# Performance work log

Hardware: AMD Instinct MI355X
Metric: run time of the kernel (lower is better)

## Reference

```python
import jax, jax.numpy as jnp
import numpy as np
from jax import lax

DN = ('NCDHW', 'OIDHW', 'NCDHW')

def _reflect_conv(s, w, pad_dhw):
    # s: [B,2,D,H,W]; reflect-pad spatial dims then VALID conv -> same spatial size
    p = jnp.pad(s, ((0, 0), (0, 0)) + pad_dhw, mode='reflect')
    return lax.conv_general_dilated(p, w, window_strides=(1, 1, 1),
                                    padding='VALID', dimension_numbers=DN)

def setup_inputs() -> dict:
    key = jax.random.key(0)
    k = jax.random.split(key, 5)
    x = jax.random.normal(k[0], (4, 32, 16, 128, 128), dtype=jnp.float32)
    w1 = jax.random.normal(k[1], (1, 2, 7, 7, 5), dtype=jnp.float32) * 0.1
    w2 = jax.random.normal(k[2], (1, 2, 5, 5, 3), dtype=jnp.float32) * 0.1
    w3 = jax.random.normal(k[3], (1, 2, 3, 3, 1), dtype=jnp.float32) * 0.2
    wf = jax.random.normal(k[4], (1, 3, 1, 1, 1), dtype=jnp.float32) * 0.5
    return {'x': x, 'w1': w1, 'w2': w2, 'w3': w3, 'wf': wf}

def reference(x, w1, w2, w3, wf):
    # channel pool: mean & max over channel dim -> [B,2,D,H,W]
    s_in = jnp.concatenate([jnp.mean(x, axis=1, keepdims=True),
                            jnp.max(x, axis=1, keepdims=True)], axis=1)
    # branch pads in (D,H,W) order match kernels (7,7,5)/(5,5,3)/(3,3,1)
    s1 = _reflect_conv(s_in, w1, ((3, 3), (3, 3), (2, 2)))
    s2 = _reflect_conv(s_in, w2, ((2, 2), (2, 2), (1, 1)))
    s3 = _reflect_conv(s_in, w3, ((1, 1), (1, 1), (0, 0)))
    s = jnp.concatenate([s1, s2, s3], axis=1)  # [B,3,D,H,W]
    fused = lax.conv_general_dilated(s, wf, window_strides=(1, 1, 1),
                                     padding='VALID', dimension_numbers=DN)
    spatial_weight = jax.nn.sigmoid(fused)  # [B,1,D,H,W]
    return x * spatial_weight
```

## Files before the change

kernel.cpp:

```cpp
#include <hip/hip_runtime.h>
#include <math.h>

#define B_ 4
#define C_ 32
#define D_ 16
#define H_ 128
#define W_ 128
#define HW_ (H_*W_)
#define SP_ (D_*HW_)

typedef float f32x4 __attribute__((ext_vector_type(4)));

__device__ __forceinline__ int refl(int i, int n) {
    i = (i < 0) ? -i : i;
    i = (i >= n) ? (2*n - 2 - i) : i;
    return i;
}

__global__ void prep_weights_kernel(const float* __restrict__ w1,
                                    const float* __restrict__ w2,
                                    const float* __restrict__ w3,
                                    const float* __restrict__ wf,
                                    float* __restrict__ Wc) {
    int t = blockIdx.x * blockDim.x + threadIdx.x;
    if (t >= 2*7*7*5) return;
    int ow = t % 5;
    int oh = (t / 5) % 7;
    int od = (t / 35) % 7;
    int ci = t / 245;
    float v = wf[0] * w1[((ci*7+od)*7+oh)*5+ow];
    if (od>=1 && od<=5 && oh>=1 && oh<=5 && ow>=1 && ow<=3)
        v = fmaf(wf[1], w2[((ci*5+(od-1))*5+(oh-1))*3+(ow-1)], v);
    if (od>=2 && od<=4 && oh>=2 && oh<=4 && ow==2)
        v = fmaf(wf[2], w3[(ci*3+(od-2))*3+(oh-2)], v);
    Wc[t] = v;
}

__global__ __launch_bounds__(256) void pool_kernel(const float* __restrict__ x,
                                                   float* __restrict__ s) {
    int t = blockIdx.x * blockDim.x + threadIdx.x;
    if (t >= B_*D_*H_*(W_/4)) return;
    int w4 = (t % (W_/4)) * 4;
    int rest = t / (W_/4);
    int h = rest % H_;
    int bd = rest / H_;
    int d = bd % D_;
    int b = bd / D_;
    const float* xp = x + (b*C_*D_ + d)*HW_ + h*W_ + w4;
    f32x4 v = *(const f32x4*)xp;
    float sx=v.x, sy=v.y, sz=v.z, sw=v.w;
    float mx=v.x, my=v.y, mz=v.z, mw=v.w;
    #pragma unroll 4
    for (int c = 1; c < C_; ++c) {
        f32x4 u = *(const f32x4*)(xp + c*SP_);
        sx+=u.x; sy+=u.y; sz+=u.z; sw+=u.w;
        mx=fmaxf(mx,u.x); my=fmaxf(my,u.y); mz=fmaxf(mz,u.z); mw=fmaxf(mw,u.w);
    }
    const float inv = 1.0f/32.0f;
    float* sm = s + ((b*2+0)*D_ + d)*HW_ + h*W_ + w4;
    float* sM = s + ((b*2+1)*D_ + d)*HW_ + h*W_ + w4;
    f32x4 a; a.x=sx*inv; a.y=sy*inv; a.z=sz*inv; a.w=sw*inv;
    f32x4 m; m.x=mx; m.y=my; m.z=mz; m.w=mw;
    *(f32x4*)sm = a;
    *(f32x4*)sM = m;
}

__global__ __launch_bounds__(256) void spatial_att_kernel(
        const float* __restrict__ x,
        const float* __restrict__ s,
        const float* __restrict__ Wc,
        float* __restrict__ out) {
    int bid = blockIdx.x;
    int ht = bid & 15;
    int d0 = (bid >> 4) & 15;
    int b  = bid >> 8;
    int t = threadIdx.x;
    int lane = t & 63;
    int w0 = (t & 31) * 4;
    int h0 = ht * 8 + (t >> 5);

    const bool le = (t & 31) == 0;
    const bool re = (t & 31) == 31;

    int drow[7];
    #pragma unroll
    for (int od = 0; od < 7; ++od) drow[od] = refl(d0 + od - 3, D_) * HW_;

    float acc[4] = {0.f, 0.f, 0.f, 0.f};

    for (int ci = 0; ci < 2; ++ci) {
        const float* sc = s + (b*2 + ci)*SP_;
        const float* wcb_ci = Wc + ci*245;
        for (int oh = 0; oh < 7; ++oh) {
            const float* sh = sc + refl(h0 + oh - 3, H_)*W_ + w0;
            const float* wcb = wcb_ci + oh*5;
            #pragma unroll
            for (int od = 0; od < 7; ++od) {
                const f32x4 vv = *(const f32x4*)(sh + drow[od]);
                float lz = __shfl(vv.z, lane - 1);
                float lw = __shfl(vv.w, lane - 1);
                float rx = __shfl(vv.x, lane + 1);
                float ry = __shfl(vv.y, lane + 1);
                float v[8];
                v[0] = le ? vv.z : lz;
                v[1] = le ? vv.y : lw;
                v[2] = vv.x; v[3] = vv.y; v[4] = vv.z; v[5] = vv.w;
                v[6] = re ? vv.z : rx;
                v[7] = re ? vv.y : ry;
                const float* wp = wcb + od*35;
                #pragma unroll
                for (int ow = 0; ow < 5; ++ow) {
                    float wgt = wp[ow];
                    #pragma unroll
                    for (int wi = 0; wi < 4; ++wi)
                        acc[wi] = fmaf(wgt, v[wi+ow], acc[wi]);
                }
            }
        }
    }

    float sg[4];
    #pragma unroll
    for (int wi = 0; wi < 4; ++wi)
        sg[wi] = 1.0f/(1.0f + __expf(-acc[wi]));

    int obase = (b*C_*D_ + d0)*HW_ + h0*W_ + w0;
    #pragma unroll 4
    for (int c = 0; c < C_; ++c) {
        int i0 = obase + c*SP_;
        f32x4 xv = *(const f32x4*)(x + i0);
        f32x4 o; o.x=xv.x*sg[0]; o.y=xv.y*sg[1]; o.z=xv.z*sg[2]; o.w=xv.w*sg[3];
        __builtin_nontemporal_store(o, (f32x4*)(out + i0));
    }
}

extern "C" void kernel_launch(void* const* d_in, const int* in_sizes, int n_in,
                              void* d_out, int out_size, void* d_ws, size_t ws_size,
                              hipStream_t stream) {
    const float* x  = (const float*)d_in[0];
    const float* w1 = (const float*)d_in[1];
    const float* w2 = (const float*)d_in[2];
    const float* w3 = (const float*)d_in[3];
    const float* wf = (const float*)d_in[4];
    float* out = (float*)d_out;
    float* Wc = (float*)d_ws;
    float* s  = (float*)d_ws + 512;

    prep_weights_kernel<<<1, 512, 0, stream>>>(w1, w2, w3, wf, Wc);
    pool_kernel<<<(B_*D_*H_*(W_/4) + 255)/256, 256, 0, stream>>>(x, s);
    spatial_att_kernel<<<B_*D_*(H_/8), 256, 0, stream>>>(x, s, Wc, out);
}
```

Before: 88.57 us.

## Split stencil and multiply into separate kernels; use overlapping loads instead of shuffles

The fused stencil+multiply kernel is split in two. A stencil kernel writes a sigmoid gate map to workspace, and a separate multiply kernel spreads the 32-channel x*gate pass across 8x more blocks, so bandwidth-bound work gets more parallelism. Inside the stencil, cross-lane shuffles are replaced by two overlapping vector loads per row, and the pool loop now uses vector adds with a larger unroll. The cost is an extra launch plus a small gate-map write and read.

```diff
diff --git a/kernel.cpp b/kernel.cpp
--- a/kernel.cpp
+++ b/kernel.cpp
@@ -32,7 +32,7 @@
     if (od>=1 && od<=5 && oh>=1 && oh<=5 && ow>=1 && ow<=3)
         v = fmaf(wf[1], w2[((ci*5+(od-1))*5+(oh-1))*3+(ow-1)], v);
     if (od>=2 && od<=4 && oh>=2 && oh<=4 && ow==2)
-        v = fmaf(wf[2], w3[(ci*3+(od-2))*3+(oh-2)], v);
+        v = fmaf(wf[2], w3[(ci*3+(od-2))*3+(ow==2?(oh-2):0)], v);
     Wc[t] = v;
 }
 
@@ -48,39 +48,34 @@
     int b = bd / D_;
     const float* xp = x + (b*C_*D_ + d)*HW_ + h*W_ + w4;
     f32x4 v = *(const f32x4*)xp;
-    float sx=v.x, sy=v.y, sz=v.z, sw=v.w;
-    float mx=v.x, my=v.y, mz=v.z, mw=v.w;
-    #pragma unroll 4
+    f32x4 sm = v, mx = v;
+    #pragma unroll 8
     for (int c = 1; c < C_; ++c) {
         f32x4 u = *(const f32x4*)(xp + c*SP_);
-        sx+=u.x; sy+=u.y; sz+=u.z; sw+=u.w;
-        mx=fmaxf(mx,u.x); my=fmaxf(my,u.y); mz=fmaxf(mz,u.z); mw=fmaxf(mw,u.w);
+        sm += u;
+        mx.x=fmaxf(mx.x,u.x); mx.y=fmaxf(mx.y,u.y); mx.z=fmaxf(mx.z,u.z); mx.w=fmaxf(mx.w,u.w);
     }
-    const float inv = 1.0f/32.0f;
-    float* sm = s + ((b*2+0)*D_ + d)*HW_ + h*W_ + w4;
-    float* sM = s + ((b*2+1)*D_ + d)*HW_ + h*W_ + w4;
-    f32x4 a; a.x=sx*inv; a.y=sy*inv; a.z=sz*inv; a.w=sw*inv;
-    f32x4 m; m.x=mx; m.y=my; m.z=mz; m.w=mw;
-    *(f32x4*)sm = a;
-    *(f32x4*)sM = m;
+    sm *= (1.0f/32.0f);
+    *(f32x4*)(s + ((b*2+0)*D_ + d)*HW_ + h*W_ + w4) = sm;
+    *(f32x4*)(s + ((b*2+1)*D_ + d)*HW_ + h*W_ + w4) = mx;
 }
 
-__global__ __launch_bounds__(256) void spatial_att_kernel(
-        const float* __restrict__ x,
+__global__ __launch_bounds__(256) void stencil_kernel(
         const float* __restrict__ s,
         const float* __restrict__ Wc,
-        float* __restrict__ out) {
+        float* __restrict__ sg) {
     int bid = blockIdx.x;
     int ht = bid & 15;
     int d0 = (bid >> 4) & 15;
     int b  = bid >> 8;
     int t = threadIdx.x;
-    int lane = t & 63;
     int w0 = (t & 31) * 4;
     int h0 = ht * 8 + (t >> 5);
 
     const bool le = (t & 31) == 0;
     const bool re = (t & 31) == 31;
+    const int offL = le ? 0 : -2;
+    const int offR = re ? 0 :  2;
 
     int drow[7];
     #pragma unroll
@@ -96,17 +91,18 @@
             const float* wcb = wcb_ci + oh*5;
             #pragma unroll
             for (int od = 0; od < 7; ++od) {
-                const f32x4 vv = *(const f32x4*)(sh + drow[od]);
-                float lz = __shfl(vv.z, lane - 1);
-                float lw = __shfl(vv.w, lane - 1);
-                float rx = __shfl(vv.x, lane + 1);
-                float ry = __shfl(vv.y, lane + 1);
+                const float* rp = sh + drow[od];
+                const f32x4 L = *(const f32x4*)(rp + offL);
+                const f32x4 R = *(const f32x4*)(rp + offR);
                 float v[8];
-                v[0] = le ? vv.z : lz;
-                v[1] = le ? vv.y : lw;
-                v[2] = vv.x; v[3] = vv.y; v[4] = vv.z; v[5] = vv.w;
-                v[6] = re ? vv.z : rx;
-                v[7] = re ? vv.y : ry;
+                v[0] = le ? L.z : L.x;
+                v[1] = L.y;
+                v[2] = le ? L.x : L.z;
+                v[3] = le ? L.y : L.w;
+                v[4] = re ? R.z : R.x;
+                v[5] = re ? R.w : R.y;
+                v[6] = R.z;
+                v[7] = re ? R.y : R.w;
                 const float* wp = wcb + od*35;
                 #pragma unroll
                 for (int ow = 0; ow < 5; ++ow) {
@@ -119,18 +115,35 @@
         }
     }
 
-    float sg[4];
+    f32x4 o;
+    o.x = 1.0f/(1.0f + __expf(-acc[0]));
+    o.y = 1.0f/(1.0f + __expf(-acc[1]));
+    o.z = 1.0f/(1.0f + __expf(-acc[2]));
+    o.w = 1.0f/(1.0f + __expf(-acc[3]));
+    *(f32x4*)(sg + ((b*D_ + d0)*H_ + h0)*W_ + w0) = o;
+}
+
+__global__ __launch_bounds__(256) void mult_kernel(
+        const float* __restrict__ x,
+        const float* __restrict__ sg,
+        float* __restrict__ out) {
+    int bid = blockIdx.x;
+    int h = bid & 127;
+    int d = (bid >> 7) & 15;
+    int b = bid >> 11;
+    int t = threadIdx.x;
+    int w4 = (t & 31) * 4;
+    int c0 = t >> 5;
+
+    f32x4 g = *(const f32x4*)(sg + ((b*D_ + d)*H_ + h)*W_ + w4);
+
+    int base = (b*C_*D_ + d)*HW_ + h*W_ + w4;
     #pragma unroll
-    for (int wi = 0; wi < 4; ++wi)
-        sg[wi] = 1.0f/(1.0f + __expf(-acc[wi]));
-
-    int obase = (b*C_*D_ + d0)*HW_ + h0*W_ + w0;
-    #pragma unroll 4
-    for (int c = 0; c < C_; ++c) {
-        int i0 = obase + c*SP_;
+    for (int k = 0; k < 4; ++k) {
+        int c = c0 + k*8;
+        int i0 = base + c*SP_;
         f32x4 xv = *(const f32x4*)(x + i0);
-        f32x4 o; o.x=xv.x*sg[0]; o.y=xv.y*sg[1]; o.z=xv.z*sg[2]; o.w=xv.w*sg[3];
-        __builtin_nontemporal_store(o, (f32x4*)(out + i0));
+        __builtin_nontemporal_store(xv * g, (f32x4*)(out + i0));
     }
 }
 
@@ -145,8 +158,10 @@
     float* out = (float*)d_out;
     float* Wc = (float*)d_ws;
     float* s  = (float*)d_ws + 512;
+    float* sg = s + B_*2*SP_;
 
     prep_weights_kernel<<<1, 512, 0, stream>>>(w1, w2, w3, wf, Wc);
     pool_kernel<<<(B_*D_*H_*(W_/4) + 255)/256, 256, 0, stream>>>(x, s);
-    spatial_att_kernel<<<B_*D_*(H_/8), 256, 0, stream>>>(x, s, Wc, out);
+    stencil_kernel<<<B_*D_*(H_/8), 256, 0, stream>>>(s, Wc, sg);
+    mult_kernel<<<B_*D_*H_, 256, 0, stream>>>(x, sg, out);
 }
```

Result: slower. 115.4 us (+30.3%).
